# Kernel tuning notes

Hardware: AMD Instinct MI355X
Metric: run time of the kernel (lower is better)

Reference implementation:

```python
import jax, jax.numpy as jnp
import numpy as np

EPS = 1e-5

def conv1x1(x, w):
    # x: [B,C,T,D,H,W], w: [O,C] -> [B,O,T,D,H,W]
    return jnp.einsum('oc,bctdhw->botdhw', w, x)

def conv4d_3(x, w):
    # 3x3x3x3 4D conv, padding=1, stride=1, decomposed as 3 shifted 3D convs.
    # x: [B,C,T,D,H,W], w: [O,C,3,3,3,3]
    B, C, T, D, H, W = x.shape
    O = w.shape[0]
    xp = jnp.pad(x, ((0, 0), (0, 0), (1, 1), (1, 1), (1, 1), (1, 1)))
    out = None
    for k in range(3):  # small fixed loop over first kernel dim
        xk = xp[:, :, k:k + T]                      # [B,C,T,D+2,H+2,W+2]
        xk = xk.transpose(0, 2, 1, 3, 4, 5).reshape(B * T, C, D + 2, H + 2, W + 2)
        ok = jax.lax.conv_general_dilated(
            xk, w[:, :, k], window_strides=(1, 1, 1), padding='VALID',
            dimension_numbers=('NCDHW', 'OIDHW', 'NCDHW'))  # [B*T,O,D,H,W]
        out = ok if out is None else out + ok
    return out.reshape(B, T, O, D, H, W).transpose(0, 2, 1, 3, 4, 5)

def bn4d(x, g, b):
    # BatchNorm over (B, T, D, H, W) per channel (training-mode batch stats).
    axes = (0, 2, 3, 4, 5)
    m = jnp.mean(x, axis=axes, keepdims=True)
    v = jnp.mean(jnp.square(x - m), axis=axes, keepdims=True)
    sh = (1, -1, 1, 1, 1, 1)
    return (x - m) * jax.lax.rsqrt(v + EPS) * g.reshape(sh) + b.reshape(sh)

def setup_inputs() -> dict:
    key = jax.random.key(0)
    ks = jax.random.split(key, 4)
    B, C, T, D, H, W = 2, 256, 8, 16, 16, 16
    planes = 64
    return {
        'x': jax.random.normal(ks[0], (B, C, T, D, H, W), jnp.float32),
        'w1': jax.random.normal(ks[1], (planes, C), jnp.float32) * 0.05,
        'g1': jnp.ones((planes,), jnp.float32),
        'b1': jnp.zeros((planes,), jnp.float32),
        'w2': jax.random.normal(ks[2], (planes, planes, 3, 3, 3, 3), jnp.float32) * 0.05,
        'g2': jnp.ones((planes,), jnp.float32),
        'b2': jnp.zeros((planes,), jnp.float32),
        'w3': jax.random.normal(ks[3], (4 * planes, planes), jnp.float32) * 0.05,
        'g3': jnp.ones((4 * planes,), jnp.float32),
        'b3': jnp.zeros((4 * planes,), jnp.float32),
    }

def reference(x, w1, g1, b1, w2, g2, b2, w3, g3, b3):
    out = jax.nn.relu(bn4d(conv1x1(x, w1), g1, b1))
    out = jax.nn.relu(bn4d(conv4d_3(out, w2), g2, b2))
    out = bn4d(conv1x1(out, w3), g3, b3)
    return jax.nn.relu(out + x)
```

## Files before the change

kernel.cpp:

```cpp
#include <hip/hip_runtime.h>

#define S_TOT 32768

typedef unsigned short ushortT;
typedef __attribute__((ext_vector_type(8))) short short8;
typedef __attribute__((ext_vector_type(4))) float floatx4;

__device__ __forceinline__ ushortT f2bf(float f) {
    unsigned u = __float_as_uint(f);
    u = (u + 0x7fffu + ((u >> 16) & 1u)) >> 16;
    return (ushortT)u;
}
__device__ __forceinline__ float bf2f(ushortT h) {
    return __uint_as_float(((unsigned)h) << 16);
}

__global__ __launch_bounds__(256) void k_prep_w(const float* __restrict__ w1,
                                                const float* __restrict__ w2,
                                                const float* __restrict__ w3,
                                                ushortT* __restrict__ wb1,
                                                ushortT* __restrict__ wb2,
                                                ushortT* __restrict__ wb3) {
    int idx = blockIdx.x * 256 + threadIdx.x;
    if (idx < 16384) {
        int e = idx;
        int j = e & 7, o = (e >> 3) & 63, q = (e >> 9) & 3, cc = e >> 11;
        int c = cc * 32 + q * 8 + j;
        wb1[e] = f2bf(w1[o * 256 + c]);
    } else if (idx < 16384 + 331776) {
        int e = idx - 16384;
        int j = e & 7, o = (e >> 3) & 63, cb = (e >> 9) & 7, tap = e >> 12;
        int c = cb * 8 + j;
        wb2[e] = f2bf(w2[((size_t)o * 64 + c) * 81 + tap]);
    } else if (idx < 16384 + 331776 + 16384) {
        int e = idx - 348160;
        int j = e & 7, o = (e >> 3) & 255, g = e >> 11;
        int ks = g >> 2, q = g & 3;
        int c = ks * 32 + q * 8 + j;
        wb3[e] = f2bf(w3[o * 64 + c]);
    }
}

__global__ __launch_bounds__(256) void k_stats_bf16(const ushortT* __restrict__ y,
                                                    int nch,
                                                    float* __restrict__ sum,
                                                    float* __restrict__ sq) {
    __shared__ float red[8];
    int ch = blockIdx.x, tid = threadIdx.x;
    float s = 0.f, q = 0.f;
    for (int b = 0; b < 2; ++b) {
        const ushortT* p = y + ((size_t)(b * nch + ch)) * S_TOT;
        for (int i = tid * 8; i < S_TOT; i += 256 * 8) {
            uint4 v = *(const uint4*)(p + i);
            uint32_t va[4] = {v.x, v.y, v.z, v.w};
#pragma unroll
            for (int k = 0; k < 4; ++k) {
                float a = bf2f((ushortT)(va[k] & 0xffffu));
                float c = bf2f((ushortT)(va[k] >> 16));
                s += a + c;
                q += a * a + c * c;
            }
        }
    }
#pragma unroll
    for (int off = 32; off; off >>= 1) {
        s += __shfl_down(s, off);
        q += __shfl_down(q, off);
    }
    int wid = tid >> 6;
    if ((tid & 63) == 0) { red[wid] = s; red[4 + wid] = q; }
    __syncthreads();
    if (tid == 0) {
        sum[ch] = red[0] + red[1] + red[2] + red[3];
        sq[ch]  = red[4] + red[5] + red[6] + red[7];
    }
}

__global__ __launch_bounds__(256) void k_stats_f32(const float* __restrict__ y,
                                                   int nch,
                                                   float* __restrict__ sum,
                                                   float* __restrict__ sq) {
    __shared__ float red[8];
    int ch = blockIdx.x, tid = threadIdx.x;
    float s = 0.f, q = 0.f;
    for (int b = 0; b < 2; ++b) {
        const float* p = y + ((size_t)(b * nch + ch)) * S_TOT;
        for (int i = tid * 4; i < S_TOT; i += 256 * 4) {
            float4 v = *(const float4*)(p + i);
            s += v.x + v.y + v.z + v.w;
            q += v.x * v.x + v.y * v.y + v.z * v.z + v.w * v.w;
        }
    }
#pragma unroll
    for (int off = 32; off; off >>= 1) {
        s += __shfl_down(s, off);
        q += __shfl_down(q, off);
    }
    int wid = tid >> 6;
    if ((tid & 63) == 0) { red[wid] = s; red[4 + wid] = q; }
    __syncthreads();
    if (tid == 0) {
        sum[ch] = red[0] + red[1] + red[2] + red[3];
        sq[ch]  = red[4] + red[5] + red[6] + red[7];
    }
}

__global__ __launch_bounds__(256) void k_conv1_mfma(const float* __restrict__ x,
                                                    const ushortT* __restrict__ wb1,
                                                    ushortT* __restrict__ y1bf) {
    __shared__ __align__(16) ushortT xb[128 * 40];

    int tid = threadIdx.x;
    int blk = blockIdx.x;
    int b  = blk >> 8;
    int n0 = (blk & 255) * 128;

    int lane = tid & 63;
    int wv   = tid >> 6;
    int m    = lane & 15;
    int q    = lane >> 4;

    int c_loc = tid & 31;
    int ng    = tid >> 5;

    floatx4 acc[8];
#pragma unroll
    for (int i = 0; i < 8; ++i) acc[i] = (floatx4){0.f, 0.f, 0.f, 0.f};

    for (int cc = 0; cc < 8; ++cc) {
        short8 afr = *(const short8*)(wb1 + (((cc * 4 + q) * 64) + wv * 16 + m) * 8);

        __syncthreads();
        {
            int c = cc * 32 + c_loc;
            const float* xp = x + ((size_t)(b * 256 + c)) * S_TOT + n0 + ng * 16;
#pragma unroll
            for (int k = 0; k < 4; ++k) {
                float4 v = *(const float4*)(xp + k * 4);
                int nb = ng * 16 + k * 4;
                xb[(nb + 0) * 40 + c_loc] = f2bf(v.x);
                xb[(nb + 1) * 40 + c_loc] = f2bf(v.y);
                xb[(nb + 2) * 40 + c_loc] = f2bf(v.z);
                xb[(nb + 3) * 40 + c_loc] = f2bf(v.w);
            }
        }
        __syncthreads();

#pragma unroll
        for (int pt = 0; pt < 8; ++pt) {
            short8 bfr = *(const short8*)(xb + (pt * 16 + m) * 40 + q * 8);
            acc[pt] = __builtin_amdgcn_mfma_f32_16x16x32_bf16(afr, bfr, acc[pt], 0, 0, 0);
        }
    }

#pragma unroll
    for (int pt = 0; pt < 8; ++pt) {
#pragma unroll
        for (int r = 0; r < 4; ++r) {
            int o = wv * 16 + q * 4 + r;
            y1bf[((size_t)(b * 64 + o)) * S_TOT + n0 + pt * 16 + m] = f2bf(acc[pt][r]);
        }
    }
}

__global__ __launch_bounds__(256) void k_prep(const ushortT* __restrict__ yin,
                                              const float* __restrict__ sum,
                                              const float* __restrict__ sq,
                                              const float* __restrict__ g,
                                              const float* __restrict__ bb,
                                              ushortT* __restrict__ yout) {
    size_t i = ((size_t)blockIdx.x * 256 + threadIdx.x) * 4;
    int c = (int)((i >> 15) & 63);
    const float n = 65536.f;
    float mean = sum[c] / n;
    float var  = sq[c] / n - mean * mean;
    float a  = g[c] * rsqrtf(var + 1e-5f);
    float bs = bb[c] - mean * a;
    ushort4 v = *(const ushort4*)(yin + i);
    ushort4 r;
    r.x = f2bf(fmaxf(a * bf2f(v.x) + bs, 0.f));
    r.y = f2bf(fmaxf(a * bf2f(v.y) + bs, 0.f));
    r.z = f2bf(fmaxf(a * bf2f(v.z) + bs, 0.f));
    r.w = f2bf(fmaxf(a * bf2f(v.w) + bs, 0.f));
    *(ushort4*)(yout + i) = r;
}

__global__ __launch_bounds__(256, 2) void k_conv2_mfma(
        const ushortT* __restrict__ y1n,
        const ushortT* __restrict__ wb2,
        ushortT* __restrict__ y2bf) {
    __shared__ __align__(16) ushortT xs[180 * 64];

    int tid = threadIdx.x;
    int blk = blockIdx.x;
    int b  = blk >> 8;
    int t  = (blk >> 5) & 7;
    int d  = (blk >> 1) & 15;
    int h0 = (blk & 1) * 8;

    int lane = tid & 63;
    int wv   = tid >> 6;
    int m    = lane & 15;
    int q    = lane >> 4;
    int wp   = wv & 1;
    int wo   = wv >> 1;

    int c2      = tid & 31;
    int prbase  = tid >> 5;

    floatx4 acc[2][4];
#pragma unroll
    for (int i = 0; i < 2; ++i)
#pragma unroll
        for (int j = 0; j < 4; ++j) acc[i][j] = (floatx4){0.f, 0.f, 0.f, 0.f};

    const size_t cstride = 32768;
    uint32_t* xsd = (uint32_t*)xs;

    for (int ktd = 0; ktd < 9; ++ktd) {
        int kt = ktd / 3, kd = ktd - kt * 3;
        int tt = t + kt - 1;
        int dd = d + kd - 1;
        bool pv = (tt >= 0 && tt < 8 && dd >= 0 && dd < 16);
        if (!pv) continue;

        short8 afr[9][2][2];
#pragma unroll
        for (int khw = 0; khw < 9; ++khw) {
            int tap = ktd * 9 + khw;
#pragma unroll
            for (int ks = 0; ks < 2; ++ks)
#pragma unroll
                for (int ot = 0; ot < 2; ++ot) {
                    afr[khw][ks][ot] = *(const short8*)(wb2 +
                        (((size_t)(tap * 8 + ks * 4 + q)) * 64 + wo * 32 + ot * 16 + m) * 8);
                }
        }

        __syncthreads();

        for (int pr = prbase; pr < 10; pr += 8) {
            int hin = h0 + pr - 1;
            uint32_t pack[18];
            if (hin >= 0 && hin < 16) {
                const ushortT* p0 = y1n +
                    (((size_t)(b * 64 + 2 * c2) * 8 + tt) * 16 + dd) * 256 + hin * 16;
                const ushortT* p1 = p0 + cstride;
                uint4 r0 = *(const uint4*)p0;
                uint4 r1 = *(const uint4*)(p0 + 8);
                uint4 s0 = *(const uint4*)p1;
                uint4 s1 = *(const uint4*)(p1 + 8);
                uint32_t ra[8] = {r0.x, r0.y, r0.z, r0.w, r1.x, r1.y, r1.z, r1.w};
                uint32_t sa[8] = {s0.x, s0.y, s0.z, s0.w, s1.x, s1.y, s1.z, s1.w};
                pack[0] = 0; pack[17] = 0;
#pragma unroll
                for (int k = 0; k < 8; ++k) {
                    pack[1 + 2 * k] = (ra[k] & 0xffffu) | (sa[k] << 16);
                    pack[2 + 2 * k] = (ra[k] >> 16) | (sa[k] & 0xffff0000u);
                }
            } else {
#pragma unroll
                for (int k = 0; k < 18; ++k) pack[k] = 0;
            }
            int pb = pr * 18;
#pragma unroll
            for (int k = 0; k < 18; ++k) {
                int ppos = pb + k;
                xsd[ppos * 32 + ((((c2 >> 2) ^ (ppos & 7)) << 2) | (c2 & 3))] = pack[k];
            }
        }
        __syncthreads();

#pragma unroll
        for (int kh = 0; kh < 3; ++kh) {
#pragma unroll
            for (int kw = 0; kw < 3; ++kw) {
                int khw = kh * 3 + kw;
#pragma unroll
                for (int nt = 0; nt < 4; ++nt) {
                    int ppos = (wp * 4 + nt + kh) * 18 + m + kw;
                    int sw = (ppos & 7);
                    const ushortT* row = xs + ppos * 64;
                    short8 b0 = *(const short8*)(row + (((0 * 4 + q) ^ sw) << 3));
                    short8 b1 = *(const short8*)(row + (((1 * 4 + q) ^ sw) << 3));
                    acc[0][nt] = __builtin_amdgcn_mfma_f32_16x16x32_bf16(
                        afr[khw][0][0], b0, acc[0][nt], 0, 0, 0);
                    acc[1][nt] = __builtin_amdgcn_mfma_f32_16x16x32_bf16(
                        afr[khw][0][1], b0, acc[1][nt], 0, 0, 0);
                    acc[0][nt] = __builtin_amdgcn_mfma_f32_16x16x32_bf16(
                        afr[khw][1][0], b1, acc[0][nt], 0, 0, 0);
                    acc[1][nt] = __builtin_amdgcn_mfma_f32_16x16x32_bf16(
                        afr[khw][1][1], b1, acc[1][nt], 0, 0, 0);
                }
            }
        }
    }

#pragma unroll
    for (int ot = 0; ot < 2; ++ot) {
#pragma unroll
        for (int nt = 0; nt < 4; ++nt) {
#pragma unroll
            for (int r = 0; r < 4; ++r) {
                int o  = wo * 32 + ot * 16 + q * 4 + r;
                int hh = h0 + wp * 4 + nt;
                y2bf[(((size_t)(b * 64 + o) * 8 + t) * 16 + d) * 256 + hh * 16 + m] =
                    f2bf(acc[ot][nt][r]);
            }
        }
    }
}

__global__ __launch_bounds__(256) void k_conv3_mfma(const ushortT* __restrict__ y2n,
                                                    const ushortT* __restrict__ wb3,
                                                    float* __restrict__ y3) {
    __shared__ __align__(16) ushortT yb[64 * 72];

    int tid = threadIdx.x;
    int blk = blockIdx.x;
    int b  = blk >> 9;
    int n0 = (blk & 511) * 64;

    int lane = tid & 63;
    int wv   = tid >> 6;
    int m    = lane & 15;
    int q    = lane >> 4;

    for (int idx = tid; idx < 512; idx += 256) {
        int c = idx >> 3, k = idx & 7;
        uint4 v = *(const uint4*)(y2n + ((size_t)(b * 64 + c)) * S_TOT + n0 + k * 8);
        uint32_t va[4] = {v.x, v.y, v.z, v.w};
#pragma unroll
        for (int p = 0; p < 4; ++p) {
            yb[(k * 8 + 2 * p)     * 72 + c] = (ushortT)(va[p] & 0xffffu);
            yb[(k * 8 + 2 * p + 1) * 72 + c] = (ushortT)(va[p] >> 16);
        }
    }
    __syncthreads();

    floatx4 acc[4][4];
#pragma unroll
    for (int i = 0; i < 4; ++i)
#pragma unroll
        for (int j = 0; j < 4; ++j) acc[i][j] = (floatx4){0.f, 0.f, 0.f, 0.f};

#pragma unroll
    for (int ks = 0; ks < 2; ++ks) {
        short8 afr[4];
#pragma unroll
        for (int ot = 0; ot < 4; ++ot)
            afr[ot] = *(const short8*)(wb3 +
                (((ks * 4 + q) * 256) + wv * 64 + ot * 16 + m) * 8);
#pragma unroll
        for (int pt = 0; pt < 4; ++pt) {
            short8 bfr = *(const short8*)(yb + (pt * 16 + m) * 72 + ks * 32 + q * 8);
#pragma unroll
            for (int ot = 0; ot < 4; ++ot)
                acc[ot][pt] = __builtin_amdgcn_mfma_f32_16x16x32_bf16(
                    afr[ot], bfr, acc[ot][pt], 0, 0, 0);
        }
    }

#pragma unroll
    for (int ot = 0; ot < 4; ++ot) {
#pragma unroll
        for (int pt = 0; pt < 4; ++pt) {
#pragma unroll
            for (int r = 0; r < 4; ++r) {
                int o = wv * 64 + ot * 16 + q * 4 + r;
                y3[((size_t)(b * 256 + o)) * S_TOT + n0 + pt * 16 + m] = acc[ot][pt][r];
            }
        }
    }
}

__global__ __launch_bounds__(256) void k_final(const float* __restrict__ x,
                                               const float* __restrict__ sum,
                                               const float* __restrict__ sq,
                                               const float* __restrict__ g,
                                               const float* __restrict__ bb,
                                               float* __restrict__ out) {
    size_t i = ((size_t)blockIdx.x * 256 + threadIdx.x) * 4;
    int o = (int)((i >> 15) & 255);
    const float n = 65536.f;
    float mean = sum[o] / n;
    float var  = sq[o] / n - mean * mean;
    float a  = g[o] * rsqrtf(var + 1e-5f);
    float bs = bb[o] - mean * a;
    float4 y  = *(float4*)(out + i);
    float4 xv = *(const float4*)(x + i);
    float4 r;
    r.x = fmaxf(a * y.x + bs + xv.x, 0.f);
    r.y = fmaxf(a * y.y + bs + xv.y, 0.f);
    r.z = fmaxf(a * y.z + bs + xv.z, 0.f);
    r.w = fmaxf(a * y.w + bs + xv.w, 0.f);
    *(float4*)(out + i) = r;
}

extern "C" void kernel_launch(void* const* d_in, const int* in_sizes, int n_in,
                              void* d_out, int out_size, void* d_ws, size_t ws_size,
                              hipStream_t stream) {
    const float* x  = (const float*)d_in[0];
    const float* w1 = (const float*)d_in[1];
    const float* g1 = (const float*)d_in[2];
    const float* b1 = (const float*)d_in[3];
    const float* w2 = (const float*)d_in[4];
    const float* g2 = (const float*)d_in[5];
    const float* b2 = (const float*)d_in[6];
    const float* w3 = (const float*)d_in[7];
    const float* g3 = (const float*)d_in[8];
    const float* b3 = (const float*)d_in[9];

    char* ws = (char*)d_ws;
    ushortT* y1bf = (ushortT*)(ws);
    ushortT* y1n  = (ushortT*)(ws + 8388608);
    ushortT* y2bf = (ushortT*)(ws + 16777216);
    ushortT* y2n  = (ushortT*)(ws + 25165824);
    ushortT* wb1  = (ushortT*)(ws + 33554432);
    ushortT* wb2  = (ushortT*)(ws + 33587200);
    ushortT* wb3  = (ushortT*)(ws + 34250752);
    float*   stats = (float*)(ws + 34283520);
    float* sum1 = stats;        float* sq1 = stats + 64;
    float* sum2 = stats + 128;  float* sq2 = stats + 192;
    float* sum3 = stats + 256;  float* sq3 = stats + 512;
    float* y3 = (float*)d_out;

    k_prep_w     <<<1424,  256, 0, stream>>>(w1, w2, w3, wb1, wb2, wb3);
    k_conv1_mfma <<<512,   256, 0, stream>>>(x, wb1, y1bf);
    k_stats_bf16 <<<64,    256, 0, stream>>>(y1bf, 64, sum1, sq1);
    k_prep       <<<4096,  256, 0, stream>>>(y1bf, sum1, sq1, g1, b1, y1n);
    k_conv2_mfma <<<512,   256, 0, stream>>>(y1n, wb2, y2bf);
    k_stats_bf16 <<<64,    256, 0, stream>>>(y2bf, 64, sum2, sq2);
    k_prep       <<<4096,  256, 0, stream>>>(y2bf, sum2, sq2, g2, b2, y2n);
    k_conv3_mfma <<<1024,  256, 0, stream>>>(y2n, wb3, y3);
    k_stats_f32  <<<256,   256, 0, stream>>>(y3, 256, sum3, sq3);
    k_final      <<<16384, 256, 0, stream>>>(x, sum3, sq3, g3, b3, y3);
}
```

Baseline: 269.9 us.

## Fuse BN statistics into conv epilogues and normalization into consumer loads

```diff
diff --git a/kernel.cpp b/kernel.cpp
--- a/kernel.cpp
+++ b/kernel.cpp
@@ -14,13 +14,22 @@
 __device__ __forceinline__ float bf2f(ushortT h) {
     return __uint_as_float(((unsigned)h) << 16);
 }
+__device__ __forceinline__ uint32_t nrm2(uint32_t u, float a, float bs) {
+    float lo = fmaxf(fmaf(a, bf2f((ushortT)(u & 0xffffu)), bs), 0.f);
+    float hi = fmaxf(fmaf(a, bf2f((ushortT)(u >> 16)), bs), 0.f);
+    return (uint32_t)f2bf(lo) | ((uint32_t)f2bf(hi) << 16);
+}
+
+#define NSTRIPE 8
+#define STRIDE_ST 768
 
 __global__ __launch_bounds__(256) void k_prep_w(const float* __restrict__ w1,
                                                 const float* __restrict__ w2,
                                                 const float* __restrict__ w3,
                                                 ushortT* __restrict__ wb1,
                                                 ushortT* __restrict__ wb2,
-                                                ushortT* __restrict__ wb3) {
+                                                ushortT* __restrict__ wb3,
+                                                float* __restrict__ stats) {
     int idx = blockIdx.x * 256 + threadIdx.x;
     if (idx < 16384) {
         int e = idx;
@@ -38,76 +47,15 @@
         int ks = g >> 2, q = g & 3;
         int c = ks * 32 + q * 8 + j;
         wb3[e] = f2bf(w3[o * 64 + c]);
-    }
-}
-
-__global__ __launch_bounds__(256) void k_stats_bf16(const ushortT* __restrict__ y,
-                                                    int nch,
-                                                    float* __restrict__ sum,
-                                                    float* __restrict__ sq) {
-    __shared__ float red[8];
-    int ch = blockIdx.x, tid = threadIdx.x;
-    float s = 0.f, q = 0.f;
-    for (int b = 0; b < 2; ++b) {
-        const ushortT* p = y + ((size_t)(b * nch + ch)) * S_TOT;
-        for (int i = tid * 8; i < S_TOT; i += 256 * 8) {
-            uint4 v = *(const uint4*)(p + i);
-            uint32_t va[4] = {v.x, v.y, v.z, v.w};
-#pragma unroll
-            for (int k = 0; k < 4; ++k) {
-                float a = bf2f((ushortT)(va[k] & 0xffffu));
-                float c = bf2f((ushortT)(va[k] >> 16));
-                s += a + c;
-                q += a * a + c * c;
-            }
-        }
-    }
-#pragma unroll
-    for (int off = 32; off; off >>= 1) {
-        s += __shfl_down(s, off);
-        q += __shfl_down(q, off);
-    }
-    int wid = tid >> 6;
-    if ((tid & 63) == 0) { red[wid] = s; red[4 + wid] = q; }
-    __syncthreads();
-    if (tid == 0) {
-        sum[ch] = red[0] + red[1] + red[2] + red[3];
-        sq[ch]  = red[4] + red[5] + red[6] + red[7];
-    }
-}
-
-__global__ __launch_bounds__(256) void k_stats_f32(const float* __restrict__ y,
-                                                   int nch,
-                                                   float* __restrict__ sum,
-                                                   float* __restrict__ sq) {
-    __shared__ float red[8];
-    int ch = blockIdx.x, tid = threadIdx.x;
-    float s = 0.f, q = 0.f;
-    for (int b = 0; b < 2; ++b) {
-        const float* p = y + ((size_t)(b * nch + ch)) * S_TOT;
-        for (int i = tid * 4; i < S_TOT; i += 256 * 4) {
-            float4 v = *(const float4*)(p + i);
-            s += v.x + v.y + v.z + v.w;
-            q += v.x * v.x + v.y * v.y + v.z * v.z + v.w * v.w;
-        }
-    }
-#pragma unroll
-    for (int off = 32; off; off >>= 1) {
-        s += __shfl_down(s, off);
-        q += __shfl_down(q, off);
-    }
-    int wid = tid >> 6;
-    if ((tid & 63) == 0) { red[wid] = s; red[4 + wid] = q; }
-    __syncthreads();
-    if (tid == 0) {
-        sum[ch] = red[0] + red[1] + red[2] + red[3];
-        sq[ch]  = red[4] + red[5] + red[6] + red[7];
+    } else if (idx < 364544 + NSTRIPE * STRIDE_ST) {
+        stats[idx - 364544] = 0.f;
     }
 }
 
 __global__ __launch_bounds__(256) void k_conv1_mfma(const float* __restrict__ x,
                                                     const ushortT* __restrict__ wb1,
-                                                    ushortT* __restrict__ y1bf) {
+                                                    ushortT* __restrict__ y1bf,
+                                                    float* __restrict__ stats) {
     __shared__ __align__(16) ushortT xb[128 * 40];
 
     int tid = threadIdx.x;
@@ -161,35 +109,43 @@
             y1bf[((size_t)(b * 64 + o)) * S_TOT + n0 + pt * 16 + m] = f2bf(acc[pt][r]);
         }
     }
-}
-
-__global__ __launch_bounds__(256) void k_prep(const ushortT* __restrict__ yin,
-                                              const float* __restrict__ sum,
-                                              const float* __restrict__ sq,
-                                              const float* __restrict__ g,
-                                              const float* __restrict__ bb,
-                                              ushortT* __restrict__ yout) {
-    size_t i = ((size_t)blockIdx.x * 256 + threadIdx.x) * 4;
-    int c = (int)((i >> 15) & 63);
-    const float n = 65536.f;
-    float mean = sum[c] / n;
-    float var  = sq[c] / n - mean * mean;
-    float a  = g[c] * rsqrtf(var + 1e-5f);
-    float bs = bb[c] - mean * a;
-    ushort4 v = *(const ushort4*)(yin + i);
-    ushort4 r;
-    r.x = f2bf(fmaxf(a * bf2f(v.x) + bs, 0.f));
-    r.y = f2bf(fmaxf(a * bf2f(v.y) + bs, 0.f));
-    r.z = f2bf(fmaxf(a * bf2f(v.z) + bs, 0.f));
-    r.w = f2bf(fmaxf(a * bf2f(v.w) + bs, 0.f));
-    *(ushort4*)(yout + i) = r;
+
+    float ssum[4] = {0.f, 0.f, 0.f, 0.f}, ssq[4] = {0.f, 0.f, 0.f, 0.f};
+#pragma unroll
+    for (int pt = 0; pt < 8; ++pt)
+#pragma unroll
+        for (int r = 0; r < 4; ++r) {
+            float v = acc[pt][r];
+            ssum[r] += v;
+            ssq[r]  += v * v;
+        }
+#pragma unroll
+    for (int off = 1; off < 16; off <<= 1)
+#pragma unroll
+        for (int r = 0; r < 4; ++r) {
+            ssum[r] += __shfl_xor(ssum[r], off);
+            ssq[r]  += __shfl_xor(ssq[r], off);
+        }
+    if (m == 0) {
+        float* st = stats + (blk & (NSTRIPE - 1)) * STRIDE_ST;
+#pragma unroll
+        for (int r = 0; r < 4; ++r) {
+            int o = wv * 16 + q * 4 + r;
+            atomicAdd(st + o, ssum[r]);
+            atomicAdd(st + 64 + o, ssq[r]);
+        }
+    }
 }
 
 __global__ __launch_bounds__(256, 2) void k_conv2_mfma(
-        const ushortT* __restrict__ y1n,
+        const ushortT* __restrict__ y1bf,
         const ushortT* __restrict__ wb2,
+        const float* __restrict__ g1,
+        const float* __restrict__ b1,
+        float* __restrict__ stats,
         ushortT* __restrict__ y2bf) {
     __shared__ __align__(16) ushortT xs[180 * 64];
+    __shared__ float st2[128];
 
     int tid = threadIdx.x;
     int blk = blockIdx.x;
@@ -208,6 +164,24 @@
     int c2      = tid & 31;
     int prbase  = tid >> 5;
 
+    if (tid < 128) st2[tid] = 0.f;
+
+    int c0 = 2 * c2, c1v = c0 + 1;
+    float s0 = 0.f, q0 = 0.f, s1 = 0.f, q1 = 0.f;
+#pragma unroll
+    for (int p = 0; p < NSTRIPE; ++p) {
+        const float* sp = stats + p * STRIDE_ST;
+        s0 += sp[c0];  q0 += sp[64 + c0];
+        s1 += sp[c1v]; q1 += sp[64 + c1v];
+    }
+    const float inv_n = 1.f / 65536.f;
+    float mu0 = s0 * inv_n, var0 = q0 * inv_n - mu0 * mu0;
+    float a0  = g1[c0] * rsqrtf(var0 + 1e-5f);
+    float bb0 = b1[c0] - mu0 * a0;
+    float mu1 = s1 * inv_n, var1 = q1 * inv_n - mu1 * mu1;
+    float a1  = g1[c1v] * rsqrtf(var1 + 1e-5f);
+    float bb1 = b1[c1v] - mu1 * a1;
+
     floatx4 acc[2][4];
 #pragma unroll
     for (int i = 0; i < 2; ++i)
@@ -243,15 +217,20 @@
             int hin = h0 + pr - 1;
             uint32_t pack[18];
             if (hin >= 0 && hin < 16) {
-                const ushortT* p0 = y1n +
-                    (((size_t)(b * 64 + 2 * c2) * 8 + tt) * 16 + dd) * 256 + hin * 16;
+                const ushortT* p0 = y1bf +
+                    (((size_t)(b * 64 + c0) * 8 + tt) * 16 + dd) * 256 + hin * 16;
                 const ushortT* p1 = p0 + cstride;
                 uint4 r0 = *(const uint4*)p0;
                 uint4 r1 = *(const uint4*)(p0 + 8);
-                uint4 s0 = *(const uint4*)p1;
-                uint4 s1 = *(const uint4*)(p1 + 8);
+                uint4 s0v = *(const uint4*)p1;
+                uint4 s1v = *(const uint4*)(p1 + 8);
                 uint32_t ra[8] = {r0.x, r0.y, r0.z, r0.w, r1.x, r1.y, r1.z, r1.w};
-                uint32_t sa[8] = {s0.x, s0.y, s0.z, s0.w, s1.x, s1.y, s1.z, s1.w};
+                uint32_t sa[8] = {s0v.x, s0v.y, s0v.z, s0v.w, s1v.x, s1v.y, s1v.z, s1v.w};
+#pragma unroll
+                for (int k = 0; k < 8; ++k) {
+                    ra[k] = nrm2(ra[k], a0, bb0);
+                    sa[k] = nrm2(sa[k], a1, bb1);
+                }
                 pack[0] = 0; pack[17] = 0;
 #pragma unroll
                 for (int k = 0; k < 8; ++k) {
@@ -282,15 +261,15 @@
                     int sw = (ppos & 7);
                     const ushortT* row = xs + ppos * 64;
                     short8 b0 = *(const short8*)(row + (((0 * 4 + q) ^ sw) << 3));
-                    short8 b1 = *(const short8*)(row + (((1 * 4 + q) ^ sw) << 3));
+                    short8 b1f = *(const short8*)(row + (((1 * 4 + q) ^ sw) << 3));
                     acc[0][nt] = __builtin_amdgcn_mfma_f32_16x16x32_bf16(
                         afr[khw][0][0], b0, acc[0][nt], 0, 0, 0);
                     acc[1][nt] = __builtin_amdgcn_mfma_f32_16x16x32_bf16(
                         afr[khw][0][1], b0, acc[1][nt], 0, 0, 0);
                     acc[0][nt] = __builtin_amdgcn_mfma_f32_16x16x32_bf16(
-                        afr[khw][1][0], b1, acc[0][nt], 0, 0, 0);
+                        afr[khw][1][0], b1f, acc[0][nt], 0, 0, 0);
                     acc[1][nt] = __builtin_amdgcn_mfma_f32_16x16x32_bf16(
-                        afr[khw][1][1], b1, acc[1][nt], 0, 0, 0);
+                        afr[khw][1][1], b1f, acc[1][nt], 0, 0, 0);
                 }
             }
         }
@@ -309,10 +288,49 @@
             }
         }
     }
-}
-
-__global__ __launch_bounds__(256) void k_conv3_mfma(const ushortT* __restrict__ y2n,
+
+    float ss[2][4], sqv[2][4];
+#pragma unroll
+    for (int ot = 0; ot < 2; ++ot)
+#pragma unroll
+        for (int r = 0; r < 4; ++r) {
+            float s = 0.f, qv = 0.f;
+#pragma unroll
+            for (int nt = 0; nt < 4; ++nt) {
+                float v = acc[ot][nt][r];
+                s += v; qv += v * v;
+            }
+            ss[ot][r] = s; sqv[ot][r] = qv;
+        }
+#pragma unroll
+    for (int off = 1; off < 16; off <<= 1)
+#pragma unroll
+        for (int ot = 0; ot < 2; ++ot)
+#pragma unroll
+            for (int r = 0; r < 4; ++r) {
+                ss[ot][r]  += __shfl_xor(ss[ot][r], off);
+                sqv[ot][r] += __shfl_xor(sqv[ot][r], off);
+            }
+    if (m == 0) {
+#pragma unroll
+        for (int ot = 0; ot < 2; ++ot)
+#pragma unroll
+            for (int r = 0; r < 4; ++r) {
+                int o = wo * 32 + ot * 16 + q * 4 + r;
+                atomicAdd(&st2[o], ss[ot][r]);
+                atomicAdd(&st2[64 + o], sqv[ot][r]);
+            }
+    }
+    __syncthreads();
+    if (tid < 128)
+        atomicAdd(stats + (blk & (NSTRIPE - 1)) * STRIDE_ST + 128 + tid, st2[tid]);
+}
+
+__global__ __launch_bounds__(256) void k_conv3_mfma(const ushortT* __restrict__ y2bf,
                                                     const ushortT* __restrict__ wb3,
+                                                    const float* __restrict__ g2,
+                                                    const float* __restrict__ b2,
+                                                    float* __restrict__ stats,
                                                     float* __restrict__ y3) {
     __shared__ __align__(16) ushortT yb[64 * 72];
 
@@ -326,14 +344,26 @@
     int m    = lane & 15;
     int q    = lane >> 4;
 
+    const float inv_n = 1.f / 65536.f;
     for (int idx = tid; idx < 512; idx += 256) {
         int c = idx >> 3, k = idx & 7;
-        uint4 v = *(const uint4*)(y2n + ((size_t)(b * 64 + c)) * S_TOT + n0 + k * 8);
+        float s = 0.f, qv = 0.f;
+#pragma unroll
+        for (int p = 0; p < NSTRIPE; ++p) {
+            const float* sp = stats + p * STRIDE_ST;
+            s += sp[128 + c]; qv += sp[192 + c];
+        }
+        float mu = s * inv_n, var = qv * inv_n - mu * mu;
+        float a  = g2[c] * rsqrtf(var + 1e-5f);
+        float bs = b2[c] - mu * a;
+        uint4 v = *(const uint4*)(y2bf + ((size_t)(b * 64 + c)) * S_TOT + n0 + k * 8);
         uint32_t va[4] = {v.x, v.y, v.z, v.w};
 #pragma unroll
         for (int p = 0; p < 4; ++p) {
-            yb[(k * 8 + 2 * p)     * 72 + c] = (ushortT)(va[p] & 0xffffu);
-            yb[(k * 8 + 2 * p + 1) * 72 + c] = (ushortT)(va[p] >> 16);
+            float lo = fmaxf(fmaf(a, bf2f((ushortT)(va[p] & 0xffffu)), bs), 0.f);
+            float hi = fmaxf(fmaf(a, bf2f((ushortT)(va[p] >> 16)), bs), 0.f);
+            yb[(k * 8 + 2 * p)     * 72 + c] = f2bf(lo);
+            yb[(k * 8 + 2 * p + 1) * 72 + c] = f2bf(hi);
         }
     }
     __syncthreads();
@@ -372,19 +402,58 @@
             }
         }
     }
+
+    float ssum[4][4], ssq[4][4];
+#pragma unroll
+    for (int ot = 0; ot < 4; ++ot)
+#pragma unroll
+        for (int r = 0; r < 4; ++r) {
+            float s = 0.f, qv = 0.f;
+#pragma unroll
+            for (int pt = 0; pt < 4; ++pt) {
+                float v = acc[ot][pt][r];
+                s += v; qv += v * v;
+            }
+            ssum[ot][r] = s; ssq[ot][r] = qv;
+        }
+#pragma unroll
+    for (int off = 1; off < 16; off <<= 1)
+#pragma unroll
+        for (int ot = 0; ot < 4; ++ot)
+#pragma unroll
+            for (int r = 0; r < 4; ++r) {
+                ssum[ot][r] += __shfl_xor(ssum[ot][r], off);
+                ssq[ot][r]  += __shfl_xor(ssq[ot][r], off);
+            }
+    if (m == 0) {
+        float* st = stats + (blk & (NSTRIPE - 1)) * STRIDE_ST;
+#pragma unroll
+        for (int ot = 0; ot < 4; ++ot)
+#pragma unroll
+            for (int r = 0; r < 4; ++r) {
+                int o = wv * 64 + ot * 16 + q * 4 + r;
+                atomicAdd(st + 256 + o, ssum[ot][r]);
+                atomicAdd(st + 512 + o, ssq[ot][r]);
+            }
+    }
 }
 
 __global__ __launch_bounds__(256) void k_final(const float* __restrict__ x,
-                                               const float* __restrict__ sum,
-                                               const float* __restrict__ sq,
+                                               const float* __restrict__ stats,
                                                const float* __restrict__ g,
                                                const float* __restrict__ bb,
                                                float* __restrict__ out) {
     size_t i = ((size_t)blockIdx.x * 256 + threadIdx.x) * 4;
-    int o = (int)((i >> 15) & 255);
+    int o = (int)((blockIdx.x >> 5) & 255);
+    float s = 0.f, qv = 0.f;
+#pragma unroll
+    for (int p = 0; p < NSTRIPE; ++p) {
+        s  += stats[p * STRIDE_ST + 256 + o];
+        qv += stats[p * STRIDE_ST + 512 + o];
+    }
     const float n = 65536.f;
-    float mean = sum[o] / n;
-    float var  = sq[o] / n - mean * mean;
+    float mean = s / n;
+    float var  = qv / n - mean * mean;
     float a  = g[o] * rsqrtf(var + 1e-5f);
     float bs = bb[o] - mean * a;
     float4 y  = *(float4*)(out + i);
@@ -413,26 +482,16 @@
 
     char* ws = (char*)d_ws;
     ushortT* y1bf = (ushortT*)(ws);
-    ushortT* y1n  = (ushortT*)(ws + 8388608);
-    ushortT* y2bf = (ushortT*)(ws + 16777216);
-    ushortT* y2n  = (ushortT*)(ws + 25165824);
-    ushortT* wb1  = (ushortT*)(ws + 33554432);
-    ushortT* wb2  = (ushortT*)(ws + 33587200);
-    ushortT* wb3  = (ushortT*)(ws + 34250752);
-    float*   stats = (float*)(ws + 34283520);
-    float* sum1 = stats;        float* sq1 = stats + 64;
-    float* sum2 = stats + 128;  float* sq2 = stats + 192;
-    float* sum3 = stats + 256;  float* sq3 = stats + 512;
+    ushortT* y2bf = (ushortT*)(ws + 8388608);
+    ushortT* wb1  = (ushortT*)(ws + 16777216);
+    ushortT* wb2  = (ushortT*)(ws + 16809984);
+    ushortT* wb3  = (ushortT*)(ws + 17473536);
+    float*   stats = (float*)(ws + 17506304);
     float* y3 = (float*)d_out;
 
-    k_prep_w     <<<1424,  256, 0, stream>>>(w1, w2, w3, wb1, wb2, wb3);
-    k_conv1_mfma <<<512,   256, 0, stream>>>(x, wb1, y1bf);
-    k_stats_bf16 <<<64,    256, 0, stream>>>(y1bf, 64, sum1, sq1);
-    k_prep       <<<4096,  256, 0, stream>>>(y1bf, sum1, sq1, g1, b1, y1n);
-    k_conv2_mfma <<<512,   256, 0, stream>>>(y1n, wb2, y2bf);
-    k_stats_bf16 <<<64,    256, 0, stream>>>(y2bf, 64, sum2, sq2);
-    k_prep       <<<4096,  256, 0, stream>>>(y2bf, sum2, sq2, g2, b2, y2n);
-    k_conv3_mfma <<<1024,  256, 0, stream>>>(y2n, wb3, y3);
-    k_stats_f32  <<<256,   256, 0, stream>>>(y3, 256, sum3, sq3);
-    k_final      <<<16384, 256, 0, stream>>>(x, sum3, sq3, g3, b3, y3);
-}
+    k_prep_w     <<<1448,  256, 0, stream>>>(w1, w2, w3, wb1, wb2, wb3, stats);
+    k_conv1_mfma <<<512,   256, 0, stream>>>(x, wb1, y1bf, stats);
+    k_conv2_mfma <<<512,   256, 0, stream>>>(y1bf, wb2, g1, b1, stats, y2bf);
+    k_conv3_mfma <<<1024,  256, 0, stream>>>(y2bf, wb3, g2, b2, stats, y3);
+    k_final      <<<16384, 256, 0, stream>>>(x, stats, g3, b3, y3);
+}
```

New measurement: 262.3 us. 1.03x faster.
